# Kernel optimization log

Measured on AMD Instinct MI355X. Metric: run time of the kernel, lower is better.

Reference implementation:

```python
import jax, jax.numpy as jnp
import numpy as np

SB_EPSILON = 0.1
SB_SIZE = 1

B, S, L = 16, 256, 24


def _shift(x, axis, k):
    """y[..., i, ...] = x[..., i + k, ...], zero-padded out of range."""
    if k == 0:
        return x
    n = x.shape[axis]
    if k > 0:
        body = jax.lax.slice_in_dim(x, k, n, axis=axis)
        pad = jnp.zeros_like(jax.lax.slice_in_dim(x, 0, k, axis=axis))
        return jnp.concatenate([body, pad], axis=axis)
    k = -k
    body = jax.lax.slice_in_dim(x, 0, n - k, axis=axis)
    pad = jnp.zeros_like(jax.lax.slice_in_dim(x, 0, k, axis=axis))
    return jnp.concatenate([pad, body], axis=axis)


def setup_inputs() -> dict:
    key = jax.random.key(0)
    k1, k2 = jax.random.split(key)
    predict = jax.random.normal(k1, (B, S, S, L), dtype=jnp.float32)
    target = (jax.random.uniform(k2, (B, S, S, L)) < 0.002).astype(jnp.float32)
    # valid spans: end >= start
    tri = (jnp.arange(S)[None, :] >= jnp.arange(S)[:, None]).astype(jnp.int32)
    mask = jnp.broadcast_to(tri[None, :, :, None], (B, S, S, L)).astype(jnp.int32)
    # keep targets only on valid spans
    target = target * mask.astype(jnp.float32)
    return {"predict": predict, "target": target, "mask": mask}


def reference(predict, target, mask):
    dt = predict.dtype
    P = (target == 1).astype(dt)            # positive spans [B,S,S,L]
    M = (mask == 1).astype(dt)              # valid-span mask
    # subtract full epsilon from each positive span
    b2l = jnp.where(target == 1, target - SB_EPSILON, target)
    for dist in range(1, SB_SIZE + 1):
        eps = SB_EPSILON / (SB_SIZE * dist * 4)
        cnt = jnp.zeros_like(P)   # num valid neighbors per positive span
        add = jnp.zeros_like(P)   # smoothing mass scattered onto neighbors
        # NOTE: original code offsets neighbors by sb_size (not dist); identical for sb_size=1
        for axis, k in ((2, SB_SIZE), (2, -SB_SIZE), (1, SB_SIZE), (1, -SB_SIZE)):
            cnt = cnt + _shift(M, axis, k)          # neighbor in range and mask==1
            add = add + _shift(P, axis, -k)         # positives scattering into this cell
        b2l = b2l + eps * (add * M + P * (dist * 4 - cnt))
    # masked BCE-with-logits, mean over mask==1 elements
    x, t = predict, b2l
    bce = jnp.maximum(x, 0) - x * t + jnp.log1p(jnp.exp(-jnp.abs(x)))
    denom = jnp.sum(M)
    return jnp.sum(bce * M) / denom
```

## Files before the change

### kernel.cpp

```cpp
#include <hip/hip_runtime.h>


#define SS 256
#define LL 24

constexpr float EPS4      = 0.025f;
constexpr float INV_DENOM = 1.0f / 12632064.0f;
constexpr int   NT        = 256;
constexpr int   NB        = 16 * 128;
constexpr int   TOTAL6    = 257 * 6;

__device__ __forceinline__ float bce_term(float x, float t) {
    float ax = fabsf(x);
    return fmaxf(x, 0.f) - x * t + __logf(1.f + __expf(-ax));
}

__global__ __launch_bounds__(NT) void bs_pair(const float4* __restrict__ pred4,
                                              const float4* __restrict__ targ4,
                                              const float*  __restrict__ predf,
                                              float* __restrict__ out) {
    const int b  = blockIdx.x >> 7;
    const int iA = blockIdx.x & 127;
    const int iB = 255 - iA;
    const int lenA6 = (SS - iA) * 6;
    const int qA = (((b << 8) + iA) * SS + iA) * 6;
    const int qB = (((b << 8) + iB) * SS + iB) * 6;

    float acc  = 0.f;
    float corr = 0.f;

    for (int v = threadIdx.x; v < TOTAL6; v += NT) {
        bool inA = v < lenA6;
        int  q   = inA ? (qA + v) : (qB + (v - lenA6));

        float4 x = pred4[q];
        float4 t = targ4[q];

        acc += bce_term(x.x, t.x);
        acc += bce_term(x.y, t.y);
        acc += bce_term(x.z, t.z);
        acc += bce_term(x.w, t.w);

        if (t.x == 1.f || t.y == 1.f || t.z == 1.f || t.w == 1.f) {
            int vloc = inA ? v : (v - lenA6);
            int i    = inA ? iA : iB;
            int j    = i + vloc / 6;
            bool hasL = j > i;
            bool hasR = j < SS - 1;
            bool hasU = i > 0;
            float cnt = (hasL ? 2.f : 0.f) + (hasR ? 1.f : 0.f) + (hasU ? 1.f : 0.f);
            int ebase = q * 4;
            float tv[4] = {t.x, t.y, t.z, t.w};
            float xv[4] = {x.x, x.y, x.z, x.w};
#pragma unroll
            for (int k = 0; k < 4; ++k) {
                if (tv[k] == 1.f) {
                    int e = ebase + k;
                    float s = 0.f;
                    if (hasL) s += predf[e - LL];
                    if (hasR) s += predf[e + LL];
                    if (hasU) s += predf[e - LL * SS];
                    if (hasL) s += predf[e + LL * SS];
                    corr += s - xv[k] * cnt;
                }
            }
        }
    }

    float vsum = fmaf(-EPS4, corr, acc);

#pragma unroll
    for (int off = 32; off; off >>= 1) vsum += __shfl_down(vsum, off, 64);
    __shared__ float s[NT / 64];
    int w = threadIdx.x >> 6;
    if ((threadIdx.x & 63) == 0) s[w] = vsum;
    __syncthreads();
    if (threadIdx.x == 0) {
        float bsum = 0.f;
#pragma unroll
        for (int k = 0; k < NT / 64; ++k) bsum += s[k];
        atomicAdd(out, bsum * INV_DENOM);
    }
}

extern "C" void kernel_launch(void* const* d_in, const int* in_sizes, int n_in,
                              void* d_out, int out_size, void* d_ws, size_t ws_size,
                              hipStream_t stream) {
    const float4* pred4 = (const float4*)d_in[0];
    const float4* targ4 = (const float4*)d_in[1];
    const float*  predf = (const float*)d_in[0];
    float* out = (float*)d_out;

    hipMemsetAsync(out, 0, sizeof(float), stream);
    bs_pair<<<NB, NT, 0, stream>>>(pred4, targ4, predf, out);
}
```

Baseline: 254.4 us.

## Software-prefetch next float4 pair and replace atomics with two-stage reduction

The main loop now issues the loads for the next iteration before computing the BCE terms on the current values, so memory latency can overlap with arithmetic. The single global atomicAdd per block and the memset are replaced by per-block partial sums written to workspace, then summed by a one-block final kernel. This adds a second kernel launch and extra registers for the prefetched values, in exchange for fewer stalls and no atomic contention.

```diff
diff --git a/kernel.cpp b/kernel.cpp
--- a/kernel.cpp
+++ b/kernel.cpp
@@ -18,7 +18,7 @@
 __global__ __launch_bounds__(NT) void bs_pair(const float4* __restrict__ pred4,
                                               const float4* __restrict__ targ4,
                                               const float*  __restrict__ predf,
-                                              float* __restrict__ out) {
+                                              float* __restrict__ partial) {
     const int b  = blockIdx.x >> 7;
     const int iA = blockIdx.x & 127;
     const int iB = 255 - iA;
@@ -29,12 +29,21 @@
     float acc  = 0.f;
     float corr = 0.f;
 
-    for (int v = threadIdx.x; v < TOTAL6; v += NT) {
-        bool inA = v < lenA6;
-        int  q   = inA ? (qA + v) : (qB + (v - lenA6));
+    int v = threadIdx.x;
+    int q = (v < lenA6) ? (qA + v) : (qB + (v - lenA6));
+    float4 x = pred4[q];
+    float4 t = targ4[q];
 
-        float4 x = pred4[q];
-        float4 t = targ4[q];
+    for (;;) {
+        int  vn = v + NT;
+        bool more = vn < TOTAL6;
+        int qn = 0;
+        float4 xn, tn;
+        if (more) {
+            qn = (vn < lenA6) ? (qA + vn) : (qB + (vn - lenA6));
+            xn = pred4[qn];
+            tn = targ4[qn];
+        }
 
         acc += bce_term(x.x, t.x);
         acc += bce_term(x.y, t.y);
@@ -42,8 +51,8 @@
         acc += bce_term(x.w, t.w);
 
         if (t.x == 1.f || t.y == 1.f || t.z == 1.f || t.w == 1.f) {
-            int vloc = inA ? v : (v - lenA6);
-            int i    = inA ? iA : iB;
+            int vloc = (v < lenA6) ? v : (v - lenA6);
+            int i    = (v < lenA6) ? iA : iB;
             int j    = i + vloc / 6;
             bool hasL = j > i;
             bool hasR = j < SS - 1;
@@ -65,6 +74,9 @@
                 }
             }
         }
+
+        if (!more) break;
+        v = vn; q = qn; x = xn; t = tn;
     }
 
     float vsum = fmaf(-EPS4, corr, acc);
@@ -79,8 +91,23 @@
         float bsum = 0.f;
 #pragma unroll
         for (int k = 0; k < NT / 64; ++k) bsum += s[k];
-        atomicAdd(out, bsum * INV_DENOM);
+        partial[blockIdx.x] = bsum;
     }
+}
+
+__global__ __launch_bounds__(256) void bs_final(const float* __restrict__ partial,
+                                                float* __restrict__ out) {
+    float acc = 0.f;
+#pragma unroll
+    for (int k = threadIdx.x; k < NB; k += 256) acc += partial[k];
+#pragma unroll
+    for (int off = 32; off; off >>= 1) acc += __shfl_down(acc, off, 64);
+    __shared__ float s[4];
+    int w = threadIdx.x >> 6;
+    if ((threadIdx.x & 63) == 0) s[w] = acc;
+    __syncthreads();
+    if (threadIdx.x == 0)
+        out[0] = (s[0] + s[1] + s[2] + s[3]) * INV_DENOM;
 }
 
 extern "C" void kernel_launch(void* const* d_in, const int* in_sizes, int n_in,
@@ -89,8 +116,9 @@
     const float4* pred4 = (const float4*)d_in[0];
     const float4* targ4 = (const float4*)d_in[1];
     const float*  predf = (const float*)d_in[0];
-    float* out = (float*)d_out;
+    float* partial = (float*)d_ws;
+    float* out     = (float*)d_out;
 
-    hipMemsetAsync(out, 0, sizeof(float), stream);
-    bs_pair<<<NB, NT, 0, stream>>>(pred4, targ4, predf, out);
+    bs_pair <<<NB, NT, 0, stream>>>(pred4, targ4, predf, partial);
+    bs_final<<<1, 256, 0, stream>>>(partial, out);
 }
```

Result: faster. 239.9 us (-5.7%).
